# Kernel optimization log

Hardware: AMD Instinct MI355X
Metric: run time of the kernel (lower is better)

## Reference

```python
import jax, jax.numpy as jnp
import numpy as np

L = 16
F = 2
N_MIN = 16.0
N_MAX = 524288.0
T = 524288  # 2**19
N_PTS = 2097152  # 2**21


def setup_inputs() -> dict:
    key = jax.random.key(0)
    k1, k2 = jax.random.split(key)
    x = jax.random.uniform(k1, (N_PTS,), dtype=jnp.float32, minval=-1.0, maxval=1.0)
    hash_table = jax.random.uniform(k2, (T, F), dtype=jnp.float32, minval=-0.001, maxval=0.001)
    return {"x": x, "hash_table": hash_table, "bound": 1}


def reference(x, hash_table, bound):
    # normalize coords to [0, 1]
    xn = (x + bound) / (2.0 * bound)
    # per-level geometric growth factor b
    b = jnp.exp((jnp.log(jnp.float32(N_MAX)) - jnp.log(jnp.float32(N_MIN))) / (L - 1))
    scales = N_MIN * b ** jnp.arange(L, dtype=jnp.float32) - 1.0  # [L]
    x_scaled = xn[:, None] * scales[None, :] + 0.5                # [N, L]
    indices = jnp.floor(x_scaled).astype(jnp.int32) % T           # [N, L]
    # gather per-level features and flatten: [N, L, F] -> [N, L*F]
    return hash_table[indices].reshape(x.shape[0], -1)
```

## Files before the change

kernel.cpp:

```cpp
#include <hip/hip_runtime.h>


constexpr int T_SIZE = 524288;
constexpr int N_PTS  = 2097152;
constexpr int SLOTS  = N_PTS * 8;
constexpr int KI     = 4;
constexpr int NTH    = SLOTS / KI;

typedef float vfloat4 __attribute__((ext_vector_type(4)));

__device__ __forceinline__ float scale_for_level(int l) {
    unsigned bits = ((130u + (unsigned)l) << 23)
                  | (0x800000u - (0x100000u >> l) - (unsigned)l);
    return __uint_as_float(bits);
}

__global__ __launch_bounds__(256) void hash_encode_kernel(
    const float* __restrict__ x,
    const float* __restrict__ table,
    const int* __restrict__ bound_p,
    float* __restrict__ out)
{
    int tid = blockIdx.x * 256 + threadIdx.x;

    int j  = tid & 7;
    int l0 = j << 1;
    float s0 = scale_for_level(l0);
    float s1 = scale_for_level(l0 + 1);

    float fb  = (float)bound_p[0];
    float fb2 = __fmul_rn(2.0f, fb);

    float xv[KI];
#pragma unroll
    for (int k = 0; k < KI; ++k) {
        int n = (tid + k * NTH) >> 3;
        xv[k] = __builtin_nontemporal_load(&x[n]);
    }

    int i0[KI], i1[KI];
#pragma unroll
    for (int k = 0; k < KI; ++k) {
        float xn  = __fdiv_rn(__fadd_rn(xv[k], fb), fb2);
        float xs0 = __fadd_rn(__fmul_rn(xn, s0), 0.5f);
        float xs1 = __fadd_rn(__fmul_rn(xn, s1), 0.5f);
        i0[k] = ((int)xs0) & (T_SIZE - 1);
        i1[k] = ((int)xs1) & (T_SIZE - 1);
    }

    const float2* t2 = (const float2*)table;
    float2 a[KI], b[KI];
#pragma unroll
    for (int k = 0; k < KI; ++k) {
        a[k] = t2[i0[k]];
        b[k] = t2[i1[k]];
    }

#pragma unroll
    for (int k = 0; k < KI; ++k) {
        vfloat4 o;
        o.x = a[k].x; o.y = a[k].y; o.z = b[k].x; o.w = b[k].y;
        __builtin_nontemporal_store(o, (vfloat4*)out + (tid + k * NTH));
    }
}

extern "C" void kernel_launch(void* const* d_in, const int* in_sizes, int n_in,
                              void* d_out, int out_size, void* d_ws, size_t ws_size,
                              hipStream_t stream) {
    const float* x     = (const float*)d_in[0];
    const float* table = (const float*)d_in[1];
    const int*   bound = (const int*)d_in[2];
    float* out = (float*)d_out;

    int blocks = NTH / 256;
    hash_encode_kernel<<<blocks, 256, 0, stream>>>(x, table, bound, out);
}
```

Before: 338.4 us.

## Bin points by coordinate into buckets before gathering to localize table accesses

```diff
diff --git a/kernel.cpp b/kernel.cpp
--- a/kernel.cpp
+++ b/kernel.cpp
@@ -3,9 +3,10 @@
 
 constexpr int T_SIZE = 524288;
 constexpr int N_PTS  = 2097152;
-constexpr int SLOTS  = N_PTS * 8;
-constexpr int KI     = 4;
-constexpr int NTH    = SLOTS / KI;
+constexpr int NB     = 256;
+constexpr int CAP    = 10240;
+constexpr int CSTR   = 32;
+constexpr size_t WS_NEED = 32768 + (size_t)NB * CAP * 8;
 
 typedef float vfloat4 __attribute__((ext_vector_type(4)));
 
@@ -15,28 +16,114 @@
     return __uint_as_float(bits);
 }
 
-__global__ __launch_bounds__(256) void hash_encode_kernel(
+__global__ void k0_init(int* __restrict__ cursor) {
+    int b = threadIdx.x;
+    cursor[b * CSTR] = b * CAP;
+}
+
+__global__ __launch_bounds__(1024) void k1_bin(
+    const float* __restrict__ x,
+    const int* __restrict__ bound_p,
+    int* __restrict__ cursor,
+    uint2* __restrict__ pairs)
+{
+    __shared__ int lhist[NB];
+    __shared__ int lbase[NB];
+    int t = threadIdx.x;
+    if (t < NB) lhist[t] = 0;
+    __syncthreads();
+
+    float fb  = (float)bound_p[0];
+    float fb2 = __fmul_rn(2.0f, fb);
+    int base = blockIdx.x * 8192;
+
+    unsigned xb[8]; int bk[8]; int lr[8];
+#pragma unroll
+    for (int i = 0; i < 8; ++i) {
+        int n = base + t + i * 1024;
+        float xv = x[n];
+        xb[i] = __float_as_uint(xv);
+        float xn = __fdiv_rn(__fadd_rn(xv, fb), fb2);
+        int b = (int)(xn * 256.0f);
+        b = b < 0 ? 0 : (b > 255 ? 255 : b);
+        bk[i] = b;
+        lr[i] = atomicAdd(&lhist[b], 1);
+    }
+    __syncthreads();
+    if (t < NB) lbase[t] = atomicAdd(&cursor[t * CSTR], lhist[t]);
+    __syncthreads();
+#pragma unroll
+    for (int i = 0; i < 8; ++i) {
+        int n = base + t + i * 1024;
+        int pos = lbase[bk[i]] + lr[i];
+        pairs[pos] = make_uint2(xb[i], (unsigned)n);
+    }
+}
+
+__global__ __launch_bounds__(1024) void k2_main(
+    const uint2* __restrict__ pairs,
+    const int* __restrict__ cursor,
+    const float* __restrict__ table,
+    const int* __restrict__ bound_p,
+    float* __restrict__ out)
+{
+    unsigned bid = blockIdx.x;
+    unsigned swz = (bid & 7u) * (20480u / 8u) + (bid >> 3);
+
+    unsigned tid  = swz * 1024u + threadIdx.x;
+    unsigned slot = tid >> 3;
+    int j = tid & 7;
+
+    int b      = (int)(slot / (unsigned)CAP);
+    int within = (int)(slot - (unsigned)b * CAP);
+    int cnt    = cursor[b * CSTR] - b * CAP;
+    if (within >= cnt) return;
+
+    uint2 pr = pairs[slot];
+    float xv   = __uint_as_float(pr.x);
+    unsigned n = pr.y;
+
+    float fb  = (float)bound_p[0];
+    float fb2 = __fmul_rn(2.0f, fb);
+    float xn  = __fdiv_rn(__fadd_rn(xv, fb), fb2);
+
+    float s0 = scale_for_level(j << 1);
+    float s1 = scale_for_level((j << 1) + 1);
+    float xs0 = __fadd_rn(__fmul_rn(xn, s0), 0.5f);
+    float xs1 = __fadd_rn(__fmul_rn(xn, s1), 0.5f);
+    int i0 = ((int)xs0) & (T_SIZE - 1);
+    int i1 = ((int)xs1) & (T_SIZE - 1);
+
+    const float2* t2 = (const float2*)table;
+    float2 a = t2[i0];
+    float2 c = t2[i1];
+
+    vfloat4 o;
+    o.x = a.x; o.y = a.y; o.z = c.x; o.w = c.y;
+    __builtin_nontemporal_store(o, (vfloat4*)out + ((n << 3) | (unsigned)j));
+}
+
+constexpr int SLOTS = N_PTS * 8;
+constexpr int KI    = 4;
+constexpr int NTH   = SLOTS / KI;
+
+__global__ __launch_bounds__(256) void hash_encode_r4(
     const float* __restrict__ x,
     const float* __restrict__ table,
     const int* __restrict__ bound_p,
     float* __restrict__ out)
 {
     int tid = blockIdx.x * 256 + threadIdx.x;
-
     int j  = tid & 7;
-    int l0 = j << 1;
-    float s0 = scale_for_level(l0);
-    float s1 = scale_for_level(l0 + 1);
-
+    float s0 = scale_for_level(j << 1);
+    float s1 = scale_for_level((j << 1) + 1);
     float fb  = (float)bound_p[0];
     float fb2 = __fmul_rn(2.0f, fb);
 
     float xv[KI];
 #pragma unroll
-    for (int k = 0; k < KI; ++k) {
-        int n = (tid + k * NTH) >> 3;
-        xv[k] = __builtin_nontemporal_load(&x[n]);
-    }
+    for (int k = 0; k < KI; ++k)
+        xv[k] = __builtin_nontemporal_load(&x[(tid + k * NTH) >> 3]);
 
     int i0[KI], i1[KI];
 #pragma unroll
@@ -51,10 +138,7 @@
     const float2* t2 = (const float2*)table;
     float2 a[KI], b[KI];
 #pragma unroll
-    for (int k = 0; k < KI; ++k) {
-        a[k] = t2[i0[k]];
-        b[k] = t2[i1[k]];
-    }
+    for (int k = 0; k < KI; ++k) { a[k] = t2[i0[k]]; b[k] = t2[i1[k]]; }
 
 #pragma unroll
     for (int k = 0; k < KI; ++k) {
@@ -72,6 +156,14 @@
     const int*   bound = (const int*)d_in[2];
     float* out = (float*)d_out;
 
-    int blocks = NTH / 256;
-    hash_encode_kernel<<<blocks, 256, 0, stream>>>(x, table, bound, out);
+    if (ws_size >= WS_NEED && d_ws != nullptr) {
+        int*   cursor = (int*)d_ws;
+        uint2* pairs  = (uint2*)((char*)d_ws + 32768);
+        k0_init<<<1, NB, 0, stream>>>(cursor);
+        k1_bin<<<N_PTS / 8192, 1024, 0, stream>>>(x, bound, cursor, pairs);
+        k2_main<<<(NB * CAP * 8) / 1024, 1024, 0, stream>>>(
+            pairs, cursor, table, bound, out);
+    } else {
+        hash_encode_r4<<<NTH / 256, 256, 0, stream>>>(x, table, bound, out);
+    }
 }
```

Measured after the change: 343.1 us. About the same (+1.4%).

## Precompute per-finest-cell records to coalesce high-level hash gathers

Applied to the files above, without the earlier changes.

```diff
diff --git a/kernel.cpp b/kernel.cpp
--- a/kernel.cpp
+++ b/kernel.cpp
@@ -5,7 +5,8 @@
 constexpr int N_PTS  = 2097152;
 constexpr int SLOTS  = N_PTS * 8;
 constexpr int KI     = 4;
-constexpr int NTH    = SLOTS / KI;
+constexpr unsigned REC_N = 524288;
+constexpr size_t REC_BYTES = (size_t)REC_N * 128;
 
 typedef float vfloat4 __attribute__((ext_vector_type(4)));
 
@@ -15,28 +16,152 @@
     return __uint_as_float(bits);
 }
 
-__global__ __launch_bounds__(256) void hash_encode_kernel(
+__device__ __forceinline__ float prev2(float f) {
+    if (!(f > 0.0f)) return 0.0f;
+    return __uint_as_float(__float_as_uint(f) - 2u);
+}
+
+__global__ __launch_bounds__(256) void k_build(
+    const float* __restrict__ table, float* __restrict__ rec)
+{
+    __shared__ float smem[256 * 32];
+    int t = threadIdx.x;
+    unsigned u = blockIdx.x * 256u + (unsigned)t;
+
+    float s15  = scale_for_level(15);
+    float xnlo = prev2(__fdiv_rn((float)u - 0.5f, s15));
+
+    float* r = &smem[t * 32];
+    const float2* t2 = (const float2*)table;
+#pragma unroll
+    for (int l = 11; l <= 14; ++l) {
+        float sl = scale_for_level(l);
+        int iA = (int)__fadd_rn(__fmul_rn(xnlo, sl), 0.5f);
+        int iB = iA + 1; if (iB > T_SIZE - 1) iB = T_SIZE - 1;
+        float2 eA = t2[iA], eB = t2[iB];
+        int k = l - 11;
+        r[k * 4 + 0] = eA.x; r[k * 4 + 1] = eA.y;
+        r[k * 4 + 2] = eB.x; r[k * 4 + 3] = eB.y;
+        ((int*)r)[18 + k] = iA;
+    }
+    float2 e15 = t2[u];
+    r[16] = e15.x; r[17] = e15.y;
+#pragma unroll
+    for (int w = 22; w < 32; ++w) r[w] = 0.0f;
+    __syncthreads();
+
+    vfloat4* dst = (vfloat4*)rec + (size_t)blockIdx.x * 2048;
+    const vfloat4* src = (const vfloat4*)smem;
+#pragma unroll
+    for (int m = 0; m < 8; ++m) dst[t + m * 256] = src[t + m * 256];
+}
+
+__global__ __launch_bounds__(256) void k_main(
     const float* __restrict__ x,
     const float* __restrict__ table,
     const int* __restrict__ bound_p,
-    float* __restrict__ out)
+    float* __restrict__ out,
+    const float* __restrict__ rec,
+    int base, int nth)
 {
-    int tid = blockIdx.x * 256 + threadIdx.x;
-
-    int j  = tid & 7;
-    int l0 = j << 1;
-    float s0 = scale_for_level(l0);
-    float s1 = scale_for_level(l0 + 1);
-
+    int tid   = blockIdx.x * 256 + threadIdx.x;
+    int slot0 = base + tid;
+    int j  = slot0 & 7;
+    float s0  = scale_for_level(j << 1);
+    float s1  = scale_for_level((j << 1) + 1);
+    float s15 = scale_for_level(15);
     float fb  = (float)bound_p[0];
     float fb2 = __fmul_rn(2.0f, fb);
 
+    float xn[KI]; int i0[KI], i1[KI];
+#pragma unroll
+    for (int k = 0; k < KI; ++k) {
+        int slot = slot0 + k * nth;
+        float xv = __builtin_nontemporal_load(&x[slot >> 3]);
+        xn[k] = __fdiv_rn(__fadd_rn(xv, fb), fb2);
+        float xs0 = __fadd_rn(__fmul_rn(xn[k], s0), 0.5f);
+        float xs1 = __fadd_rn(__fmul_rn(xn[k], s1), 0.5f);
+        i0[k] = ((int)xs0) & (T_SIZE - 1);
+        i1[k] = ((int)xs1) & (T_SIZE - 1);
+    }
+
+    const float2* t2 = (const float2*)table;
+    float2 a[KI], b[KI];
+    if (j <= 4) {
+#pragma unroll
+        for (int k = 0; k < KI; ++k) { a[k] = t2[i0[k]]; b[k] = t2[i1[k]]; }
+    } else if (j == 5) {
+#pragma unroll
+        for (int k = 0; k < KI; ++k) {
+            a[k] = t2[i0[k]];
+            unsigned u = ((unsigned)(int)__fadd_rn(__fmul_rn(xn[k], s15), 0.5f))
+                         & (T_SIZE - 1);
+            const char* rb = (const char*)rec + ((size_t)u << 7);
+            vfloat4 w = *(const vfloat4*)(rb);
+            int iA = *(const int*)(rb + 72);
+            int s = i1[k] - iA;
+            b[k] = (s == 0) ? make_float2(w.x, w.y)
+                 : (s == 1) ? make_float2(w.z, w.w)
+                 : t2[i1[k]];
+        }
+    } else if (j == 6) {
+#pragma unroll
+        for (int k = 0; k < KI; ++k) {
+            unsigned u = ((unsigned)(int)__fadd_rn(__fmul_rn(xn[k], s15), 0.5f))
+                         & (T_SIZE - 1);
+            const char* rb = (const char*)rec + ((size_t)u << 7);
+            vfloat4 w0 = *(const vfloat4*)(rb + 16);
+            vfloat4 w1 = *(const vfloat4*)(rb + 32);
+            int iA12 = *(const int*)(rb + 76);
+            int iA13 = *(const int*)(rb + 80);
+            int sA = i0[k] - iA12, sB = i1[k] - iA13;
+            a[k] = (sA == 0) ? make_float2(w0.x, w0.y)
+                 : (sA == 1) ? make_float2(w0.z, w0.w) : t2[i0[k]];
+            b[k] = (sB == 0) ? make_float2(w1.x, w1.y)
+                 : (sB == 1) ? make_float2(w1.z, w1.w) : t2[i1[k]];
+        }
+    } else {
+#pragma unroll
+        for (int k = 0; k < KI; ++k) {
+            unsigned u = (unsigned)i1[k];
+            const char* rb = (const char*)rec + ((size_t)u << 7);
+            vfloat4 w   = *(const vfloat4*)(rb + 48);
+            float2 e15  = *(const float2*)(rb + 64);
+            int iA14 = *(const int*)(rb + 84);
+            int sA = i0[k] - iA14;
+            a[k] = (sA == 0) ? make_float2(w.x, w.y)
+                 : (sA == 1) ? make_float2(w.z, w.w) : t2[i0[k]];
+            b[k] = e15;
+        }
+    }
+
+#pragma unroll
+    for (int k = 0; k < KI; ++k) {
+        vfloat4 o;
+        o.x = a[k].x; o.y = a[k].y; o.z = b[k].x; o.w = b[k].y;
+        __builtin_nontemporal_store(o, (vfloat4*)out + (slot0 + k * nth));
+    }
+}
+
+__global__ __launch_bounds__(256) void k_direct(
+    const float* __restrict__ x,
+    const float* __restrict__ table,
+    const int* __restrict__ bound_p,
+    float* __restrict__ out,
+    int base, int nth)
+{
+    int tid   = blockIdx.x * 256 + threadIdx.x;
+    int slot0 = base + tid;
+    int j = slot0 & 7;
+    float s0 = scale_for_level(j << 1);
+    float s1 = scale_for_level((j << 1) + 1);
+    float fb  = (float)bound_p[0];
+    float fb2 = __fmul_rn(2.0f, fb);
+
     float xv[KI];
 #pragma unroll
-    for (int k = 0; k < KI; ++k) {
-        int n = (tid + k * NTH) >> 3;
-        xv[k] = __builtin_nontemporal_load(&x[n]);
-    }
+    for (int k = 0; k < KI; ++k)
+        xv[k] = __builtin_nontemporal_load(&x[(slot0 + k * nth) >> 3]);
 
     int i0[KI], i1[KI];
 #pragma unroll
@@ -51,16 +176,13 @@
     const float2* t2 = (const float2*)table;
     float2 a[KI], b[KI];
 #pragma unroll
-    for (int k = 0; k < KI; ++k) {
-        a[k] = t2[i0[k]];
-        b[k] = t2[i1[k]];
-    }
+    for (int k = 0; k < KI; ++k) { a[k] = t2[i0[k]]; b[k] = t2[i1[k]]; }
 
 #pragma unroll
     for (int k = 0; k < KI; ++k) {
         vfloat4 o;
         o.x = a[k].x; o.y = a[k].y; o.z = b[k].x; o.w = b[k].y;
-        __builtin_nontemporal_store(o, (vfloat4*)out + (tid + k * NTH));
+        __builtin_nontemporal_store(o, (vfloat4*)out + (slot0 + k * nth));
     }
 }
 
@@ -72,6 +194,20 @@
     const int*   bound = (const int*)d_in[2];
     float* out = (float*)d_out;
 
-    int blocks = NTH / 256;
-    hash_encode_kernel<<<blocks, 256, 0, stream>>>(x, table, bound, out);
-}
+    if (d_ws != nullptr && ws_size >= REC_BYTES) {
+        float* rec = (float*)d_ws;
+        k_build<<<REC_N / 256, 256, 0, stream>>>(table, rec);
+        int nth = SLOTS / KI;
+        k_main<<<nth / 256, 256, 0, stream>>>(x, table, bound, out, rec, 0, nth);
+    } else {
+        constexpr int TAIL_SLOTS = 1 << 22;
+        float* rec = out + (size_t)(SLOTS - TAIL_SLOTS) * 4;
+        k_build<<<REC_N / 256, 256, 0, stream>>>(table, rec);
+        int mainslots = SLOTS - TAIL_SLOTS;
+        int nth_m = mainslots / KI;
+        k_main<<<nth_m / 256, 256, 0, stream>>>(x, table, bound, out, rec, 0, nth_m);
+        int nth_t = TAIL_SLOTS / KI;
+        k_direct<<<nth_t / 256, 256, 0, stream>>>(x, table, bound, out,
+                                                  SLOTS - TAIL_SLOTS, nth_t);
+    }
+}
```

New measurement: 373.7 us. 10.4% more time.
